# Optimization experiments

Measured on AMD Instinct MI355X. Metric: run time of the kernel, lower is better.

## Reference

```python
import jax, jax.numpy as jnp
import numpy as np

S_SRC, S_TGT, B = 64, 48, 2048
SRC, TGT, E, H = 256, 256, 512, 1024
NEG = -1e30  # stands in for -inf mask on pad/start classes (identical softmax in fp32)


def setup_inputs() -> dict:
    key = jax.random.key(0)
    ks = jax.random.split(key, 16)
    def p(k, shape):
        return jax.random.normal(k, shape, jnp.float32) * 0.02
    # padding_idx=0 -> embedding row 0 is zeros
    enc_emb = p(ks[0], (SRC, E)).at[0].set(0.0)
    dec_emb = p(ks[1], (TGT, E)).at[0].set(0.0)
    return {
        "src_seq": jax.random.randint(ks[2], (S_SRC, B), 1, SRC),
        "tgt_seq": jax.random.randint(ks[3], (S_TGT, B), 2, TGT),
        "enc_emb": enc_emb,
        "enc_Wih": p(ks[4], (3 * H, E)),
        "enc_Whh": p(ks[5], (3 * H, H)),
        "enc_bih": p(ks[6], (3 * H,)),
        "enc_bhh": p(ks[7], (3 * H,)),
        "dec_emb": dec_emb,
        "dec_Wih": p(ks[8], (3 * H, E)),
        "dec_Whh": p(ks[9], (3 * H, H)),
        "dec_bih": p(ks[10], (3 * H,)),
        "dec_bhh": p(ks[11], (3 * H,)),
        "unemb_W": p(ks[12], (TGT - 2, H)),
        "unemb_b": p(ks[13], (TGT - 2,)),
    }


def gru(x, h0, Wih, Whh, bih, bhh):
    """PyTorch-convention GRU. x: [S,B,E], h0: [B,H]. Gate order r,z,n."""
    xp = jnp.einsum('sbe,ge->sbg', x, Wih) + bih  # input projections for all steps
    def step(h, xt):
        gh = h @ Whh.T + bhh
        xr, xz, xn = jnp.split(xt, 3, axis=-1)
        hr, hz, hn = jnp.split(gh, 3, axis=-1)
        r = jax.nn.sigmoid(xr + hr)
        z = jax.nn.sigmoid(xz + hz)
        n = jnp.tanh(xn + r * hn)
        h = (1 - z) * n + z * h
        return h, h
    hT, hs = jax.lax.scan(step, h0, xp)
    return hs, hT  # [S,B,H], [B,H]


def reference(src_seq, tgt_seq, enc_emb, enc_Wih, enc_Whh, enc_bih, enc_bhh,
              dec_emb, dec_Wih, dec_Whh, dec_bih, dec_bhh, unemb_W, unemb_b):
    # ---- Encoder ----
    x0 = enc_emb[src_seq]                                   # [S_src, B, E]
    h0 = jnp.zeros((src_seq.shape[1], H), x0.dtype)
    _, h = gru(x0, h0, enc_Wih, enc_Whh, enc_bih, enc_bhh)  # [B, H]
    # ---- Decoder (training / teacher-forced path) ----
    xd = dec_emb[tgt_seq]                                   # [S_tgt, B, E]
    xs, _ = gru(xd, h, dec_Wih, dec_Whh, dec_bih, dec_bhh)  # [S_tgt, B, H]
    seq_out = jnp.einsum('sbh,vh->sbv', xs, unemb_W) + unemb_b  # [S_tgt, B, TGT-2]
    mask_cols = jnp.full(seq_out.shape[:-1] + (2,), NEG, seq_out.dtype)
    logits = jnp.concatenate([mask_cols, seq_out], axis=-1)     # [S_tgt, B, TGT]
    # labels shifted left by one; last position = 0 (ignore_index)
    labels = jnp.concatenate([tgt_seq[1:], jnp.zeros_like(tgt_seq[:1])], axis=0)
    logp = jax.nn.log_softmax(logits, axis=-1)
    nll = -jnp.take_along_axis(logp, labels[..., None], axis=-1)[..., 0]
    valid = (labels != 0).astype(nll.dtype)
    return jnp.sum(nll * valid) / jnp.sum(valid)
```

## Files before the change

kernel.cpp:

```cpp
#include <hip/hip_runtime.h>
#include <math.h>

typedef unsigned short ushort_t;
typedef __attribute__((ext_vector_type(8))) short short8;
typedef __attribute__((ext_vector_type(4))) float f32x4;

#define Bn 2048
#define Hn 1024
#define En 512
#define NSLOT 9

__device__ __forceinline__ float sigmoidf_(float x) { return 1.f / (1.f + expf(-x)); }

__device__ __forceinline__ ushort_t bf16rn(float f) {
  unsigned u = __float_as_uint(f);
  return (ushort_t)((u + 0x7FFFu + ((u >> 16) & 1u)) >> 16);
}

__device__ __forceinline__ float bf2f(ushort_t u) {
  return __uint_as_float(((unsigned)u) << 16);
}

__global__ __launch_bounds__(256) void cvt_bf16_kernel(const float* __restrict__ in,
                                                       ushort_t* __restrict__ out, int n4) {
  int i = blockIdx.x * 256 + threadIdx.x;
  if (i < n4) {
    float4 v = ((const float4*)in)[i];
    ushort4 o;
    o.x = bf16rn(v.x); o.y = bf16rn(v.y); o.z = bf16rn(v.z); o.w = bf16rn(v.w);
    ((ushort4*)out)[i] = o;
  }
}

__global__ __launch_bounds__(256) void cvt_pad_wu_kernel(const float* __restrict__ src,
                                                         ushort_t* __restrict__ dst) {
  int i = blockIdx.x * 256 + threadIdx.x;
  if (i < 256 * Hn / 4) {
    float4 v = make_float4(0.f, 0.f, 0.f, 0.f);
    if (i * 4 < 254 * Hn) v = ((const float4*)src)[i];
    ushort4 o;
    o.x = bf16rn(v.x); o.y = bf16rn(v.y); o.z = bf16rn(v.z); o.w = bf16rn(v.w);
    ((ushort4*)dst)[i] = o;
  }
}

#define GLOAD(gsrc, ldst)                                                      \
  __builtin_amdgcn_global_load_lds(                                            \
      (const __attribute__((address_space(1))) unsigned int*)(gsrc),           \
      (__attribute__((address_space(3))) unsigned int*)(ldst), 16, 0, 0)

#define PIPE_BAR(N)                                                            \
  asm volatile("s_waitcnt vmcnt(" #N ")" ::: "memory");                        \
  __builtin_amdgcn_s_barrier();                                                \
  __builtin_amdgcn_sched_barrier(0);

#define SWZ(ROW, C) ((C) ^ (((ROW) >> 1) & 3))
#define SWZ64(ROW, C) ((C) ^ ((ROW) & 7))

__global__ __launch_bounds__(256) void pgemm_kernel(
    const ushort_t* __restrict__ A,
    const ushort_t* __restrict__ Bw,
    const float* __restrict__ bias,
    float* __restrict__ P)
{
  __shared__ __align__(16) ushort_t As[64 * 32];
  __shared__ __align__(16) ushort_t Bs[64 * 32];

  const int tid = threadIdx.x;
  const int lane = tid & 63;
  const int wid = tid >> 6;
  const int wr = wid >> 1, wc = wid & 1;
  const int m0 = blockIdx.x * 64;
  const int n0 = blockIdx.y * 64;

  const int srow = tid >> 2;
  const int sseg = SWZ(srow, tid & 3) * 8;
  const ushort_t* aP = A + (size_t)(m0 + srow) * En + sseg;
  const ushort_t* bP = Bw + (size_t)(n0 + srow) * En + sseg;

  const int kc = lane >> 4;
  const int ra0 = wr * 32 + (lane & 15), ra1 = ra0 + 16;
  const int rb0 = wc * 32 + (lane & 15), rb1 = rb0 + 16;
  const int aoff0 = ra0 * 32 + SWZ(ra0, kc) * 8;
  const int aoff1 = ra1 * 32 + SWZ(ra1, kc) * 8;
  const int boff0 = rb0 * 32 + SWZ(rb0, kc) * 8;
  const int boff1 = rb1 * 32 + SWZ(rb1, kc) * 8;

  const f32x4 zero = {0.f, 0.f, 0.f, 0.f};
  f32x4 acc[2][2] = {{zero, zero}, {zero, zero}};

  for (int k0 = 0; k0 < En; k0 += 32) {
    GLOAD(aP + k0, &As[wid * 512]);
    GLOAD(bP + k0, &Bs[wid * 512]);
    asm volatile("s_waitcnt vmcnt(0)" ::: "memory");
    __syncthreads();
    short8 a0 = *(const short8*)&As[aoff0];
    short8 a1 = *(const short8*)&As[aoff1];
    short8 b0 = *(const short8*)&Bs[boff0];
    short8 b1 = *(const short8*)&Bs[boff1];
    acc[0][0] = __builtin_amdgcn_mfma_f32_16x16x32_bf16(a0, b0, acc[0][0], 0, 0, 0);
    acc[0][1] = __builtin_amdgcn_mfma_f32_16x16x32_bf16(a0, b1, acc[0][1], 0, 0, 0);
    acc[1][0] = __builtin_amdgcn_mfma_f32_16x16x32_bf16(a1, b0, acc[1][0], 0, 0, 0);
    acc[1][1] = __builtin_amdgcn_mfma_f32_16x16x32_bf16(a1, b1, acc[1][1], 0, 0, 0);
    __syncthreads();
  }

  const int colb = n0 + wc * 32 + (lane & 15);
  const int rowb = m0 + wr * 32 + ((lane >> 4) << 2);
#pragma unroll
  for (int j = 0; j < 2; ++j) {
    const int g = colb + j * 16;
    const float bv = bias[g];
#pragma unroll
    for (int i = 0; i < 2; ++i)
#pragma unroll
      for (int reg = 0; reg < 4; ++reg)
        P[(size_t)(rowb + i * 16 + reg) * 3072 + g] = acc[i][j][reg] + bv;
  }
}

#define KSTEP(BUF)                                                             \
  {                                                                            \
    short8 aF[2][2], bF[3][2];                                                 \
    _Pragma("unroll") for (int fi = 0; fi < 2; ++fi)                           \
        _Pragma("unroll") for (int h = 0; h < 2; ++h)                          \
            aF[fi][h] = *(const short8*)&As[BUF][aoff[fi][h]];                 \
    _Pragma("unroll") for (int g = 0; g < 3; ++g)                              \
        _Pragma("unroll") for (int h = 0; h < 2; ++h)                          \
            bF[g][h] = *(const short8*)&Bs[BUF][g][boff[h]];                   \
    __builtin_amdgcn_s_setprio(1);                                             \
    _Pragma("unroll") for (int h = 0; h < 2; ++h)                              \
        _Pragma("unroll") for (int g = 0; g < 3; ++g)                          \
            _Pragma("unroll") for (int fi = 0; fi < 2; ++fi)                   \
                acc[g][fi] = __builtin_amdgcn_mfma_f32_16x16x32_bf16(          \
                    aF[fi][h], bF[g][h], acc[g][fi], 0, 0, 0);                 \
    __builtin_amdgcn_s_setprio(0);                                             \
  }

#define GSTAGE(BUF, T)                                                         \
  {                                                                            \
    const int k0_ = (T) * 64;                                                  \
    GLOAD(aSrc + k0_, &As[BUF][wid * 512]);                                    \
    GLOAD(bSrc0 + k0_, &Bs[BUF][0][wid * 512]);                                \
    GLOAD(bSrc1 + k0_, &Bs[BUF][1][wid * 512]);                                \
    GLOAD(bSrc2 + k0_, &Bs[BUF][2][wid * 512]);                                \
  }

__global__ __launch_bounds__(512, 4) void gru_step_mfma(
    const int* __restrict__ seq_row,
    const float* __restrict__ P,
    const ushort_t* __restrict__ Whh,
    const float* __restrict__ bhh,
    const ushort_t* __restrict__ h_in_b,
    ushort_t* __restrict__ h_out_b)
{
  __shared__ __align__(16) ushort_t As[2][64 * 64];
  __shared__ __align__(16) ushort_t Bs[2][3][64 * 64];
  __shared__ int toks[64];

  const int tid = threadIdx.x;
  const int lane = tid & 63;
  const int wid = tid >> 6;
  const int wr = wid & 1;
  const int wc = wid >> 1;

  const int bid = blockIdx.x;
  const int q = bid & 7, t_ = bid >> 3;
  const int n0 = ((q << 1) | (t_ & 1)) * 64;
  const int m0 = (t_ >> 1) * 64;

  if (tid < 64) toks[tid] = seq_row[m0 + tid];
  __syncthreads();

  const int srow = tid >> 3;
  const int sseg = SWZ64(srow, tid & 7) * 8;

  const ushort_t* aSrc  = h_in_b + (size_t)(m0 + srow) * Hn + sseg;
  const ushort_t* bSrc0 = Whh + (size_t)(0 * Hn + n0 + srow) * Hn + sseg;
  const ushort_t* bSrc1 = Whh + (size_t)(1 * Hn + n0 + srow) * Hn + sseg;
  const ushort_t* bSrc2 = Whh + (size_t)(2 * Hn + n0 + srow) * Hn + sseg;

  const int kc = lane >> 4;
  int aoff[2][2], boff[2];
#pragma unroll
  for (int fi = 0; fi < 2; ++fi) {
    const int ra = wr * 32 + fi * 16 + (lane & 15);
#pragma unroll
    for (int h = 0; h < 2; ++h) aoff[fi][h] = ra * 64 + SWZ64(ra, h * 4 + kc) * 8;
  }
  {
    const int rb = wc * 16 + (lane & 15);
#pragma unroll
    for (int h = 0; h < 2; ++h) boff[h] = rb * 64 + SWZ64(rb, h * 4 + kc) * 8;
  }

  const f32x4 zero = {0.f, 0.f, 0.f, 0.f};
  f32x4 acc[3][2];
#pragma unroll
  for (int g = 0; g < 3; ++g)
#pragma unroll
    for (int fi = 0; fi < 2; ++fi) acc[g][fi] = zero;

  GSTAGE(0, 0);
  int buf = 0;
  for (int t = 0; t < 15; ++t) {
    GSTAGE(buf ^ 1, t + 1);
    PIPE_BAR(4)
    KSTEP(buf)
    buf ^= 1;
  }
  PIPE_BAR(0)
  KSTEP(buf)

  const int n = n0 + wc * 16 + (lane & 15);
  const int rowl = wr * 32 + ((lane >> 4) << 2);
  const float bhr = bhh[n];
  const float bhz = bhh[Hn + n];
  const float bhn = bhh[2 * Hn + n];
#pragma unroll
  for (int fi = 0; fi < 2; ++fi) {
#pragma unroll
    for (int reg = 0; reg < 4; ++reg) {
      const int lr = rowl + fi * 16 + reg;
      const int m = m0 + lr;
      const float* prow = P + (size_t)toks[lr] * 3072;
      const float xr = prow[n];
      const float xz = prow[Hn + n];
      const float xn = prow[2 * Hn + n];
      const float r = sigmoidf_(xr + acc[0][fi][reg] + bhr);
      const float z = sigmoidf_(xz + acc[1][fi][reg] + bhz);
      const float nn = tanhf(xn + r * (acc[2][fi][reg] + bhn));
      const float hv = bf2f(h_in_b[(size_t)m * Hn + n]);
      const float o = (1.f - z) * nn + z * hv;
      h_out_b[(size_t)m * Hn + n] = bf16rn(o);
    }
  }
}

#define USTAGE(BUF, T)                                                         \
  {                                                                            \
    const int k0_ = (T) * 32;                                                  \
    GLOAD(ha + k0_, AsU(BUF) + uwid * 512);                                    \
    GLOAD(w0 + k0_, BsU(BUF) + 0 * 2048 + uwid * 512);                         \
    GLOAD(w1 + k0_, BsU(BUF) + 1 * 2048 + uwid * 512);                         \
    GLOAD(w2 + k0_, BsU(BUF) + 2 * 2048 + uwid * 512);                         \
    GLOAD(w3 + k0_, BsU(BUF) + 3 * 2048 + uwid * 512);                         \
  }

#define UKSTEP(BUF)                                                            \
  {                                                                            \
    short8 a_[4], b_[4];                                                       \
    _Pragma("unroll") for (int fi = 0; fi < 4; ++fi)                           \
        a_[fi] = *(const short8*)(AsU(BUF) + uaoff[fi]);                       \
    _Pragma("unroll") for (int fj = 0; fj < 4; ++fj)                           \
        b_[fj] = *(const short8*)(BsU(BUF) + uboff[fj]);                       \
    _Pragma("unroll") for (int fi = 0; fi < 4; ++fi)                           \
        _Pragma("unroll") for (int fj = 0; fj < 4; ++fj)                       \
            acc[fi][fj] = __builtin_amdgcn_mfma_f32_16x16x32_bf16(             \
                a_[fi], b_[fj], acc[fi][fj], 0, 0, 0);                         \
  }

__global__ __launch_bounds__(256) void unembed_batched(
    const ushort_t* __restrict__ hseq,
    int s0,
    const ushort_t* __restrict__ Wp,
    const float* __restrict__ bu,
    const int* __restrict__ tgt_seq,
    double* __restrict__ loss_acc,
    unsigned long long* __restrict__ cnt_acc)
{
  __shared__ __align__(16) char usmem[16 * 1024 + 64 * 1024];
#define AsU(BUF) ((ushort_t*)usmem + (BUF) * 2048)
#define BsU(BUF) ((ushort_t*)(usmem + 16 * 1024) + (BUF) * 8192)
  float* lg = (float*)usmem;

  const int tid = threadIdx.x;
  const int lane = tid & 63;
  const int uwid = tid >> 6;

  const int step = blockIdx.x >> 5;
  const int slot = (s0 + step) % NSLOT;
  const int m0 = (blockIdx.x & 31) * 64;
  const ushort_t* h_b = hseq + (size_t)slot * Bn * Hn;
  const int* labels = tgt_seq + (size_t)(s0 + step + 1) * Bn;

  const int srow = tid >> 2;
  const int sseg = SWZ(srow, tid & 3) * 8;

  const ushort_t* ha = h_b + (size_t)(m0 + srow) * Hn + sseg;
  const ushort_t* w0 = Wp + (size_t)(0 * 64 + srow) * Hn + sseg;
  const ushort_t* w1 = Wp + (size_t)(1 * 64 + srow) * Hn + sseg;
  const ushort_t* w2 = Wp + (size_t)(2 * 64 + srow) * Hn + sseg;
  const ushort_t* w3 = Wp + (size_t)(3 * 64 + srow) * Hn + sseg;

  const int kc = lane >> 4;
  int uaoff[4], uboff[4];
#pragma unroll
  for (int fi = 0; fi < 4; ++fi) {
    const int ra = fi * 16 + (lane & 15);
    uaoff[fi] = ra * 32 + SWZ(ra, kc) * 8;
  }
#pragma unroll
  for (int fj = 0; fj < 4; ++fj) {
    const int rb = uwid * 64 + fj * 16 + (lane & 15);
    uboff[fj] = rb * 32 + SWZ(rb, kc) * 8;
  }

  const f32x4 zero = {0.f, 0.f, 0.f, 0.f};
  f32x4 acc[4][4];
#pragma unroll
  for (int fi = 0; fi < 4; ++fi)
#pragma unroll
    for (int fj = 0; fj < 4; ++fj) acc[fi][fj] = zero;

  USTAGE(0, 0);
  USTAGE(1, 1);
  USTAGE(2, 2);
  for (int t = 0; t < 29; ++t) {
    PIPE_BAR(10)
    USTAGE((t + 3) & 3, t + 3);
    UKSTEP(t & 3)
  }
  PIPE_BAR(10)
  UKSTEP(1)
  PIPE_BAR(5)
  UKSTEP(2)
  PIPE_BAR(0)
  UKSTEP(3)

  __syncthreads();
#pragma unroll
  for (int fj = 0; fj < 4; ++fj) {
    const int col = uwid * 64 + fj * 16 + (lane & 15);
    const float bv = (col < 254) ? bu[col] : 0.f;
#pragma unroll
    for (int fi = 0; fi < 4; ++fi) {
#pragma unroll
      for (int reg = 0; reg < 4; ++reg) {
        const int row = fi * 16 + (lane >> 4) * 4 + reg;
        lg[row * 256 + col] = (col < 254) ? (acc[fi][fj][reg] + bv) : -1e30f;
      }
    }
  }
  __syncthreads();

  float wsum = 0.f;
  int wcnt = 0;
#pragma unroll
  for (int rr = 0; rr < 16; ++rr) {
    const int r = uwid * 16 + rr;
    const float4 v4 = *(const float4*)&lg[r * 256 + lane * 4];
    float mx = fmaxf(fmaxf(v4.x, v4.y), fmaxf(v4.z, v4.w));
    for (int o = 32; o > 0; o >>= 1) mx = fmaxf(mx, __shfl_xor(mx, o));
    float s = expf(v4.x - mx) + expf(v4.y - mx) + expf(v4.z - mx) + expf(v4.w - mx);
    for (int o = 32; o > 0; o >>= 1) s += __shfl_xor(s, o);
    if (lane == 0) {
      const int lab = labels[m0 + r];
      if (lab != 0) {
        wsum += (logf(s) + mx) - lg[r * 256 + lab - 2];
        wcnt += 1;
      }
    }
  }
  if (lane == 0) {
    atomicAdd(loss_acc, (double)wsum);
    atomicAdd(cnt_acc, (unsigned long long)wcnt);
  }
}

__global__ void finalize_kernel(const double* __restrict__ loss_acc,
                                const unsigned long long* __restrict__ cnt_acc,
                                unsigned* __restrict__ out)
{
  unsigned long long cnt = cnt_acc[0];
  if (cnt == 0ull) cnt = 1ull;
  const float f = (float)(loss_acc[0] / (double)cnt);
  const unsigned u = __float_as_uint(f);
  const unsigned bf = (u + 0x7FFFu + ((u >> 16) & 1u)) >> 16;
  out[0] = (u & 0xFFFF0000u) | (bf & 0xFFFFu);
}

extern "C" void kernel_launch(void* const* d_in, const int* in_sizes, int n_in,
                              void* d_out, int out_size, void* d_ws, size_t ws_size,
                              hipStream_t stream)
{
  const int* src_seq = (const int*)d_in[0];
  const int* tgt_seq = (const int*)d_in[1];
  const float* enc_emb = (const float*)d_in[2];
  const float* enc_Wih = (const float*)d_in[3];
  const float* enc_Whh = (const float*)d_in[4];
  const float* enc_bih = (const float*)d_in[5];
  const float* enc_bhh = (const float*)d_in[6];
  const float* dec_emb = (const float*)d_in[7];
  const float* dec_Wih = (const float*)d_in[8];
  const float* dec_Whh = (const float*)d_in[9];
  const float* dec_bih = (const float*)d_in[10];
  const float* dec_bhh = (const float*)d_in[11];
  const float* unemb_W = (const float*)d_in[12];
  const float* unemb_b = (const float*)d_in[13];

  char* p = (char*)d_ws;
  ushort_t* hseq = (ushort_t*)p; p += (size_t)NSLOT * Bn * Hn * 2;
  ushort_t* eWih = (ushort_t*)p; p += (size_t)3 * Hn * En * 2;
  ushort_t* eWhh = (ushort_t*)p; p += (size_t)3 * Hn * Hn * 2;
  ushort_t* dWih = (ushort_t*)p; p += (size_t)3 * Hn * En * 2;
  ushort_t* dWhh = (ushort_t*)p; p += (size_t)3 * Hn * Hn * 2;
  ushort_t* eEmb = (ushort_t*)p; p += (size_t)256 * En * 2;
  ushort_t* dEmb = (ushort_t*)p; p += (size_t)256 * En * 2;
  ushort_t* Wp   = (ushort_t*)p; p += (size_t)256 * Hn * 2;
  float* Pe = (float*)p; p += (size_t)256 * 3072 * 4;
  float* Pd = (float*)p; p += (size_t)256 * 3072 * 4;
  double* loss_acc = (double*)p;
  unsigned long long* cnt_acc = (unsigned long long*)(p + 8);

  ushort_t* slot7 = hseq + (size_t)7 * Bn * Hn;
  ushort_t* slot8 = hseq + (size_t)8 * Bn * Hn;

  hipMemsetAsync(slot7, 0, (size_t)Bn * Hn * 2, stream);
  hipMemsetAsync(loss_acc, 0, 16, stream);

  struct { const float* src; ushort_t* dst; int n; } cv[6] = {
      {enc_Wih, eWih, 3 * Hn * En}, {enc_Whh, eWhh, 3 * Hn * Hn},
      {dec_Wih, dWih, 3 * Hn * En}, {dec_Whh, dWhh, 3 * Hn * Hn},
      {enc_emb, eEmb, 256 * En},    {dec_emb, dEmb, 256 * En}};
  for (int i = 0; i < 6; ++i) {
    int n4 = cv[i].n / 4;
    cvt_bf16_kernel<<<(n4 + 255) / 256, 256, 0, stream>>>(cv[i].src, cv[i].dst, n4);
  }
  cvt_pad_wu_kernel<<<(256 * Hn / 4 + 255) / 256, 256, 0, stream>>>(unemb_W, Wp);

  {
    const dim3 pg(4, 48);
    pgemm_kernel<<<pg, 256, 0, stream>>>(eEmb, eWih, enc_bih, Pe);
    pgemm_kernel<<<pg, 256, 0, stream>>>(dEmb, dWih, dec_bih, Pd);
  }

  const ushort_t* in_b = slot7;
  for (int s = 0; s < 64; ++s) {
    ushort_t* out_b = (s & 1) ? slot7 : slot8;
    gru_step_mfma<<<512, 512, 0, stream>>>(src_seq + (size_t)s * Bn, Pe, eWhh, enc_bhh,
                                           in_b, out_b);
    in_b = out_b;
  }

  int done = 0;
  for (int s = 0; s < 47; ++s) {
    const ushort_t* din_b = (s == 0) ? slot7 : hseq + (size_t)((s - 1) % NSLOT) * Bn * Hn;
    ushort_t* dout_b = hseq + (size_t)(s % NSLOT) * Bn * Hn;
    gru_step_mfma<<<512, 512, 0, stream>>>(tgt_seq + (size_t)s * Bn, Pd, dWhh, dec_bhh,
                                           din_b, dout_b);
    if (s == 7 || s == 15 || s == 23 || s == 31 || s == 39 || s == 46) {
      const int cnt = s + 1 - done;
      unembed_batched<<<cnt * 32, 256, 0, stream>>>(hseq, done, Wp, unemb_b, tgt_seq,
                                                    loss_acc, cnt_acc);
      done = s + 1;
    }
  }

  finalize_kernel<<<1, 1, 0, stream>>>(loss_acc, cnt_acc, (unsigned*)d_out);
}
```

Baseline: 2.481 ms.

## Use 32x32x16 MFMA with split-K across wave halves in GRU step

Reworks the recurrent GRU step GEMM so that each wave computes a 32x32 tile per gate with 32x32x16 bf16 MFMAs. The block's eight waves are split into two K-halves, and their partial sums are reduced through shared memory before the gate epilogue. This cuts LDS fragment loads per MFMA and uses the larger MFMA shape. In exchange it adds a shared-memory reduction and two barriers at the end. The pipeline barrier now waits for all outstanding loads after each compute step, which may reduce overlap, and only half the waves run the epilogue.

Result: slower. 3.150 ms (+27.0%).

```diff
diff --git a/kernel.cpp b/kernel.cpp
--- a/kernel.cpp
+++ b/kernel.cpp
@@ -4,6 +4,7 @@
 typedef unsigned short ushort_t;
 typedef __attribute__((ext_vector_type(8))) short short8;
 typedef __attribute__((ext_vector_type(4))) float f32x4;
+typedef __attribute__((ext_vector_type(16))) float f32x16;
 
 #define Bn 2048
 #define Hn 1024
@@ -121,29 +122,26 @@
 
 #define KSTEP(BUF)                                                             \
   {                                                                            \
-    short8 aF[2][2], bF[3][2];                                                 \
-    _Pragma("unroll") for (int fi = 0; fi < 2; ++fi)                           \
-        _Pragma("unroll") for (int h = 0; h < 2; ++h)                          \
-            aF[fi][h] = *(const short8*)&As[BUF][aoff[fi][h]];                 \
-    _Pragma("unroll") for (int g = 0; g < 3; ++g)                              \
-        _Pragma("unroll") for (int h = 0; h < 2; ++h)                          \
-            bF[g][h] = *(const short8*)&Bs[BUF][g][boff[h]];                   \
-    __builtin_amdgcn_s_setprio(1);                                             \
-    _Pragma("unroll") for (int h = 0; h < 2; ++h)                              \
-        _Pragma("unroll") for (int g = 0; g < 3; ++g)                          \
-            _Pragma("unroll") for (int fi = 0; fi < 2; ++fi)                   \
-                acc[g][fi] = __builtin_amdgcn_mfma_f32_16x16x32_bf16(          \
-                    aF[fi][h], bF[g][h], acc[g][fi], 0, 0, 0);                 \
-    __builtin_amdgcn_s_setprio(0);                                             \
+    _Pragma("unroll") for (int ks = 0; ks < 2; ++ks) {                         \
+      short8 a  = *(const short8*)(AsG(BUF) + aoff[ks]);                       \
+      short8 b0 = *(const short8*)(BsG(BUF, 0) + boff[ks]);                    \
+      short8 b1 = *(const short8*)(BsG(BUF, 1) + boff[ks]);                    \
+      short8 b2 = *(const short8*)(BsG(BUF, 2) + boff[ks]);                    \
+      __builtin_amdgcn_s_setprio(1);                                           \
+      acc0 = __builtin_amdgcn_mfma_f32_32x32x16_bf16(a, b0, acc0, 0, 0, 0);    \
+      acc1 = __builtin_amdgcn_mfma_f32_32x32x16_bf16(a, b1, acc1, 0, 0, 0);    \
+      acc2 = __builtin_amdgcn_mfma_f32_32x32x16_bf16(a, b2, acc2, 0, 0, 0);    \
+      __builtin_amdgcn_s_setprio(0);                                           \
+    }                                                                          \
   }
 
 #define GSTAGE(BUF, T)                                                         \
   {                                                                            \
     const int k0_ = (T) * 64;                                                  \
-    GLOAD(aSrc + k0_, &As[BUF][wid * 512]);                                    \
-    GLOAD(bSrc0 + k0_, &Bs[BUF][0][wid * 512]);                                \
-    GLOAD(bSrc1 + k0_, &Bs[BUF][1][wid * 512]);                                \
-    GLOAD(bSrc2 + k0_, &Bs[BUF][2][wid * 512]);                                \
+    GLOAD(aSrc + k0_, AsG(BUF) + wid * 512);                                   \
+    GLOAD(bSrc0 + k0_, BsG(BUF, 0) + wid * 512);                               \
+    GLOAD(bSrc1 + k0_, BsG(BUF, 1) + wid * 512);                               \
+    GLOAD(bSrc2 + k0_, BsG(BUF, 2) + wid * 512);                               \
   }
 
 __global__ __launch_bounds__(512, 4) void gru_step_mfma(
@@ -154,15 +152,19 @@
     const ushort_t* __restrict__ h_in_b,
     ushort_t* __restrict__ h_out_b)
 {
-  __shared__ __align__(16) ushort_t As[2][64 * 64];
-  __shared__ __align__(16) ushort_t Bs[2][3][64 * 64];
-  __shared__ int toks[64];
+  __shared__ __align__(16) char smem[16 * 1024 + 48 * 1024 + 256];
+#define AsG(BUF) ((ushort_t*)smem + (BUF) * 4096)
+#define BsG(BUF, G) ((ushort_t*)(smem + 16 * 1024) + ((BUF) * 3 + (G)) * 4096)
+  int* toks = (int*)(smem + 64 * 1024);
+  float* sc = (float*)smem;
 
   const int tid = threadIdx.x;
   const int lane = tid & 63;
   const int wid = tid >> 6;
-  const int wr = wid & 1;
-  const int wc = wid >> 1;
+  const int p = wid & 3;
+  const int pr = p & 1, pc = p >> 1;
+  const int khalf = wid >> 2;
+  const int kg = lane >> 5;
 
   const int bid = blockIdx.x;
   const int q = bid & 7, t_ = bid >> 3;
@@ -180,59 +182,76 @@
   const ushort_t* bSrc1 = Whh + (size_t)(1 * Hn + n0 + srow) * Hn + sseg;
   const ushort_t* bSrc2 = Whh + (size_t)(2 * Hn + n0 + srow) * Hn + sseg;
 
-  const int kc = lane >> 4;
-  int aoff[2][2], boff[2];
-#pragma unroll
-  for (int fi = 0; fi < 2; ++fi) {
-    const int ra = wr * 32 + fi * 16 + (lane & 15);
-#pragma unroll
-    for (int h = 0; h < 2; ++h) aoff[fi][h] = ra * 64 + SWZ64(ra, h * 4 + kc) * 8;
-  }
-  {
-    const int rb = wc * 16 + (lane & 15);
-#pragma unroll
-    for (int h = 0; h < 2; ++h) boff[h] = rb * 64 + SWZ64(rb, h * 4 + kc) * 8;
-  }
-
-  const f32x4 zero = {0.f, 0.f, 0.f, 0.f};
-  f32x4 acc[3][2];
-#pragma unroll
-  for (int g = 0; g < 3; ++g)
-#pragma unroll
-    for (int fi = 0; fi < 2; ++fi) acc[g][fi] = zero;
+  const int arow = pr * 32 + (lane & 31);
+  const int brow = pc * 32 + (lane & 31);
+  int aoff[2], boff[2];
+#pragma unroll
+  for (int ks = 0; ks < 2; ++ks) {
+    const int c = khalf * 4 + ks * 2 + kg;
+    aoff[ks] = arow * 64 + SWZ64(arow, c) * 8;
+    boff[ks] = brow * 64 + SWZ64(brow, c) * 8;
+  }
+
+  f32x16 acc0, acc1, acc2;
+#pragma unroll
+  for (int r = 0; r < 16; ++r) { acc0[r] = 0.f; acc1[r] = 0.f; acc2[r] = 0.f; }
 
   GSTAGE(0, 0);
+  PIPE_BAR(0)
   int buf = 0;
   for (int t = 0; t < 15; ++t) {
     GSTAGE(buf ^ 1, t + 1);
-    PIPE_BAR(4)
     KSTEP(buf)
+    PIPE_BAR(0)
     buf ^= 1;
   }
-  PIPE_BAR(0)
   KSTEP(buf)
 
-  const int n = n0 + wc * 16 + (lane & 15);
-  const int rowl = wr * 32 + ((lane >> 4) << 2);
-  const float bhr = bhh[n];
-  const float bhz = bhh[Hn + n];
-  const float bhn = bhh[2 * Hn + n];
-#pragma unroll
-  for (int fi = 0; fi < 2; ++fi) {
-#pragma unroll
-    for (int reg = 0; reg < 4; ++reg) {
-      const int lr = rowl + fi * 16 + reg;
+  __syncthreads();
+  if (khalf == 1) {
+#pragma unroll
+    for (int g = 0; g < 3; ++g) {
+#pragma unroll
+      for (int rq = 0; rq < 4; ++rq) {
+        const f32x16 A = (g == 0) ? acc0 : (g == 1) ? acc1 : acc2;
+        f32x4 v = {A[rq * 4 + 0], A[rq * 4 + 1], A[rq * 4 + 2], A[rq * 4 + 3]};
+        *(f32x4*)&sc[(((p * 3 + g) * 4 + rq) * 64 + lane) * 4] = v;
+      }
+    }
+  }
+  __syncthreads();
+  if (khalf == 0) {
+#pragma unroll
+    for (int g = 0; g < 3; ++g) {
+#pragma unroll
+      for (int rq = 0; rq < 4; ++rq) {
+        const f32x4 v = *(const f32x4*)&sc[(((p * 3 + g) * 4 + rq) * 64 + lane) * 4];
+#pragma unroll
+        for (int j = 0; j < 4; ++j) {
+          if (g == 0) acc0[rq * 4 + j] += v[j];
+          else if (g == 1) acc1[rq * 4 + j] += v[j];
+          else acc2[rq * 4 + j] += v[j];
+        }
+      }
+    }
+
+    const int n = n0 + pc * 32 + (lane & 31);
+    const float bhr = bhh[n];
+    const float bhz = bhh[Hn + n];
+    const float bhn = bhh[2 * Hn + n];
+#pragma unroll
+    for (int r = 0; r < 16; ++r) {
+      const int lr = pr * 32 + (r & 3) + 8 * (r >> 2) + 4 * kg;
       const int m = m0 + lr;
       const float* prow = P + (size_t)toks[lr] * 3072;
       const float xr = prow[n];
       const float xz = prow[Hn + n];
       const float xn = prow[2 * Hn + n];
-      const float r = sigmoidf_(xr + acc[0][fi][reg] + bhr);
-      const float z = sigmoidf_(xz + acc[1][fi][reg] + bhz);
-      const float nn = tanhf(xn + r * (acc[2][fi][reg] + bhn));
+      const float rg = sigmoidf_(xr + acc0[r] + bhr);
+      const float zg = sigmoidf_(xz + acc1[r] + bhz);
+      const float ng = tanhf(xn + rg * (acc2[r] + bhn));
       const float hv = bf2f(h_in_b[(size_t)m * Hn + n]);
-      const float o = (1.f - z) * nn + z * hv;
-      h_out_b[(size_t)m * Hn + n] = bf16rn(o);
+      h_out_b[(size_t)m * Hn + n] = bf16rn((1.f - zg) * ng + zg * hv);
     }
   }
 }
```
